# Performance work log

Measured on AMD Instinct MI355X. Metric: run time of the kernel, lower is better.

## Reference

```python
import jax, jax.numpy as jnp
import numpy as np
import math

H = 16        # num_heads
HD = 64       # head_dim


def get_slopes(n):
    def pow2(n):
        start = 2 ** (-2 ** (-(math.log2(n) - 3)))
        return [start * start ** i for i in range(n)]
    if math.log2(n).is_integer():
        return pow2(n)
    c = 2 ** math.floor(math.log2(n))
    return pow2(c) + get_slopes(2 * c)[0::2][: n - c]


def setup_inputs() -> dict:
    key = jax.random.key(0)
    ks = jax.random.split(key, 6)
    b, n, d = 2, 2048, 1024
    s = 1.0 / math.sqrt(d)
    return {
        "x": jax.random.normal(ks[0], (b, n, d), jnp.float32),
        "Wq": jax.random.normal(ks[1], (d, d), jnp.float32) * s,
        "Wk": jax.random.normal(ks[2], (d, d), jnp.float32) * s,
        "Wv": jax.random.normal(ks[3], (d, d), jnp.float32) * s,
        "Wo": jax.random.normal(ks[4], (d, d), jnp.float32) * s,
        "bo": jnp.zeros((d,), jnp.float32),
    }


def reference(x, Wq, Wk, Wv, Wo, bo):
    b, n, d = x.shape
    # project and split heads: [b, H, n, HD]
    def heads(w):
        return (x @ w).reshape(b, n, H, HD).transpose(0, 2, 1, 3)
    q, k, v = heads(Wq), heads(Wk), heads(Wv)

    scores = jnp.einsum("bhqd,bhkd->bhqk", q, k)  # [b,H,n,n]
    pos = jnp.arange(n)
    dist = jnp.abs(pos[None, :] - pos[:, None]).astype(scores.dtype)  # [n,n]
    slopes = jnp.asarray(get_slopes(H), dtype=scores.dtype)
    scores = scores - slopes[:, None, None] * dist  # alibi subtracted BEFORE scaling (as in source)
    causal = pos[None, :] > pos[:, None]            # upper triangle masked
    scores = jnp.where(causal, -jnp.inf, scores)
    attn = jax.nn.softmax(scores / math.sqrt(HD), axis=-1)
    ctx = jnp.einsum("bhqk,bhkd->bhqd", attn, v)
    ctx = ctx.transpose(0, 2, 1, 3).reshape(b, n, d)
    return ctx @ Wo + bo
```

## Files before the change

kernel.cpp:

```cpp
#include <hip/hip_runtime.h>
#include <hip/hip_bf16.h>
#include <stdint.h>

#define NH 16
#define HDIM 64
#define NB 2
#define NSEQ 2048
#define DM 1024
#define MROWS (NB * NSEQ)

typedef __attribute__((ext_vector_type(8))) short bf16x8;
typedef __attribute__((ext_vector_type(4))) float f32x4;

#define MFMA32(a, b, c) __builtin_amdgcn_mfma_f32_16x16x32_bf16(a, b, c, 0, 0, 0)

static __device__ __forceinline__ unsigned short f2bf(float f) {
    union { float f; unsigned u; } v;
    v.f = f;
    unsigned r = v.u + 0x7fffu + ((v.u >> 16) & 1u);
    return (unsigned short)(r >> 16);
}

static __device__ __forceinline__ unsigned pack2bf(float a, float b) {
#if __has_builtin(__builtin_amdgcn_cvt_pk_bf16_f32)
    typedef __attribute__((ext_vector_type(2))) __bf16 bf2_t;
    union { bf2_t v; unsigned u; } c;
    c.v = __builtin_amdgcn_cvt_pk_bf16_f32(a, b);
    return c.u;
#else
    return (unsigned)f2bf(a) | ((unsigned)f2bf(b) << 16);
#endif
}

static __device__ __forceinline__ float fexp2(float x) {
#if __has_builtin(__builtin_amdgcn_exp2f)
    return __builtin_amdgcn_exp2f(x);
#else
    return exp2f(x);
#endif
}

typedef __attribute__((address_space(1))) void* gas_ptr;
typedef __attribute__((address_space(3))) void* las_ptr;

static __device__ __forceinline__ void load16_lds(const void* g, void* l) {
    __builtin_amdgcn_global_load_lds((gas_ptr)(uintptr_t)g, (las_ptr)(uintptr_t)l,
                                     16, 0, 0);
}

__global__ __launch_bounds__(256) void convert_kernel(
    const float* __restrict__ x,
    const float* __restrict__ wq, const float* __restrict__ wk,
    const float* __restrict__ wv, const float* __restrict__ wo,
    unsigned short* __restrict__ xb,
    unsigned short* __restrict__ wqkvt,
    unsigned short* __restrict__ wot)
{
    __shared__ unsigned short Ts[64][66];
    int t = threadIdx.x;
    int bx = blockIdx.x;
    if (bx < 1024) {
        const float4* xs = (const float4*)x + (long)bx * 1024;
        unsigned short* xd = xb + (long)bx * 4096;
#pragma unroll
        for (int i = 0; i < 4; i++) {
            float4 v = xs[i * 256 + t];
            ushort4 o;
            o.x = f2bf(v.x); o.y = f2bf(v.y); o.z = f2bf(v.z); o.w = f2bf(v.w);
            *(ushort4*)(xd + (i * 256 + t) * 4) = o;
        }
        return;
    }
    int wi = bx - 1024;
    int wsel = wi >> 8;
    int tile = wi & 255;
    int k0 = (tile >> 4) * 64, c0 = (tile & 15) * 64;
    const float* w = (wsel == 0) ? wq : (wsel == 1) ? wk : (wsel == 2) ? wv : wo;
    int lr = t >> 6, lc = t & 63;
#pragma unroll
    for (int rr = 0; rr < 16; rr++) {
        int row = rr * 4 + lr;
        Ts[row][lc] = f2bf(w[(long)(k0 + row) * DM + c0 + lc]);
    }
    __syncthreads();
    unsigned short* dst = (wsel == 3) ? wot : (wqkvt + (long)wsel * DM * DM);
#pragma unroll
    for (int rr = 0; rr < 16; rr++) {
        int crow = rr * 4 + lr;
        dst[(long)(c0 + crow) * DM + k0 + lc] = Ts[lc][crow];
    }
}

template<int MR>
static __device__ __forceinline__ void gemm_core_db(
    const unsigned short* __restrict__ A,
    const unsigned short* __restrict__ Bt,
    int m0, int n0,
    unsigned short* __restrict__ As,
    unsigned short* __restrict__ Bs,
    f32x4 (&acc)[MR][4])
{
    constexpr int MT  = MR * 32;
    constexpr int ASZ = MT * 32;
    constexpr int BSZ = 128 * 32;
    constexpr int NA  = MT / 64;

    int t = threadIdx.x;
    int lane = t & 63;
    int wave = t >> 6;
    int l16 = lane & 15, quad = lane >> 4;
    int wm = wave >> 1, wn = wave & 1;

    const char* gA[NA];
#pragma unroll
    for (int i = 0; i < NA; i++) {
        int b = i * 256 + t;
        int row = b >> 2, g = (b & 3) ^ ((row >> 1) & 3);
        gA[i] = (const char*)(A + (long)(m0 + row) * DM) + g * 16;
    }
    const char* gB[2];
#pragma unroll
    for (int i = 0; i < 2; i++) {
        int b = i * 256 + t;
        int row = b >> 2, g = (b & 3) ^ ((row >> 1) & 3);
        gB[i] = (const char*)(Bt + (long)(n0 + row) * DM) + g * 16;
    }

    int sread = quad ^ ((l16 >> 1) & 3);
    int faOff = (wm * (MT / 2) + l16) * 32 + sread * 8;
    int fbOff = (wn * 64 + l16) * 32 + sread * 8;

#pragma unroll
    for (int i = 0; i < NA; i++)
        load16_lds(gA[i], (char*)As + i * 4096 + t * 16);
#pragma unroll
    for (int i = 0; i < 2; i++)
        load16_lds(gB[i], (char*)Bs + i * 4096 + t * 16);

    for (int kk = 0; kk < DM; kk += 32) {
        int cur = (kk >> 5) & 1;
        __syncthreads();
        if (kk + 32 < DM) {
            int nxt = cur ^ 1;
            char* abuf = (char*)(As + nxt * ASZ);
            char* bbuf = (char*)(Bs + nxt * BSZ);
#pragma unroll
            for (int i = 0; i < NA; i++)
                load16_lds(gA[i] + (kk + 32) * 2, abuf + i * 4096 + t * 16);
#pragma unroll
            for (int i = 0; i < 2; i++)
                load16_lds(gB[i] + (kk + 32) * 2, bbuf + i * 4096 + t * 16);
        }
        const unsigned short* fa = As + cur * ASZ + faOff;
        const unsigned short* fb = Bs + cur * BSZ + fbOff;
        bf16x8 af[MR], bf[4];
#pragma unroll
        for (int r = 0; r < MR; r++) af[r] = *(const bf16x8*)(fa + r * 16 * 32);
#pragma unroll
        for (int c = 0; c < 4; c++) bf[c] = *(const bf16x8*)(fb + c * 16 * 32);
#pragma unroll
        for (int r = 0; r < MR; r++)
#pragma unroll
            for (int c = 0; c < 4; c++)
                acc[r][c] = MFMA32(af[r], bf[c], acc[r][c]);
    }
}

__global__ __launch_bounds__(256, 3) void qkv_gemm_kernel(
    const unsigned short* __restrict__ A,
    const unsigned short* __restrict__ Bt,
    unsigned short* __restrict__ Qo, unsigned short* __restrict__ Ko,
    unsigned short* __restrict__ Vt)
{
    __shared__ unsigned short As[2][128 * 32];
    __shared__ unsigned short Bs[2][128 * 32];
    __shared__ unsigned short Tw[4][16][72];

    f32x4 acc[4][4] = {};
    int id = blockIdx.y * 24 + blockIdx.x;
    id = (id & 7) * 96 + (id >> 3);
    int m0 = (id / 24) * 128, n0 = (id % 24) * 128;
    gemm_core_db<4>(A, Bt, m0, n0, &As[0][0], &Bs[0][0], acc);

    int t = threadIdx.x, wave = t >> 6, lane = t & 63;
    int l16 = lane & 15, quad = lane >> 4;
    int wm = wave >> 1, wn = wave & 1;
    int rg0 = m0 + wm * 64;
    int cg0 = n0 + wn * 64;
    int z = cg0 >> 10;
    int b_ = rg0 >> 11;
    int nb0 = rg0 & (NSEQ - 1);
    int h = (cg0 & 1023) >> 6;
    long bh = (long)(b_ * NH + h);

    if (z < 2) {
        unsigned short* dst = (z == 0 ? Qo : Ko) + bh * NSEQ * HDIM;
#pragma unroll
        for (int r = 0; r < 4; r++)
#pragma unroll
            for (int reg = 0; reg < 4; reg++) {
                long rowb = (long)(nb0 + r * 16 + quad * 4 + reg) * HDIM;
#pragma unroll
                for (int c = 0; c < 4; c++)
                    dst[rowb + c * 16 + l16] = f2bf(acc[r][c][reg]);
            }
    } else {
        unsigned short* dst = Vt + bh * HDIM * NSEQ;
#pragma unroll
        for (int c = 0; c < 4; c++) {
#pragma unroll
            for (int r = 0; r < 4; r++) {
                ushort4 u;
                u.x = f2bf(acc[r][c][0]); u.y = f2bf(acc[r][c][1]);
                u.z = f2bf(acc[r][c][2]); u.w = f2bf(acc[r][c][3]);
                *(ushort4*)&Tw[wave][l16][r * 16 + quad * 4] = u;
            }
#pragma unroll
            for (int j = 0; j < 4; j++) {
                int lrow = j * 4 + quad;
                ushort4 u = *(const ushort4*)&Tw[wave][lrow][l16 * 4];
                *(ushort4*)(dst + (long)(c * 16 + lrow) * NSEQ + nb0 + l16 * 4) = u;
            }
        }
    }
}

static __device__ __forceinline__ void softmax_fixed(
    f32x4* s, bool mask, int qb, int kb, float sc2, float mrow,
    f32x4& l_vec, unsigned pbu[2][4], int l16, int quad)
{
    if (mask) {
        int fdm = qb + l16 - kb - quad * 4;
#pragma unroll
        for (int tt = 0; tt < 4; tt++)
#pragma unroll
            for (int r = 0; r < 4; r++)
                if (tt * 16 + r > fdm) s[tt][r] = -3e38f;
    }
#pragma unroll
    for (int tt = 0; tt < 4; tt++)
#pragma unroll
        for (int r = 0; r < 4; r++)
            s[tt][r] = fexp2(s[tt][r] * sc2 - mrow);
#pragma unroll
    for (int r = 0; r < 4; r++)
        l_vec[r] += (s[0][r] + s[1][r]) + (s[2][r] + s[3][r]);

#pragma unroll
    for (int p = 0; p < 2; p++) {
        pbu[p][0] = pack2bf(s[2 * p][0],     s[2 * p][1]);
        pbu[p][1] = pack2bf(s[2 * p][2],     s[2 * p][3]);
        pbu[p][2] = pack2bf(s[2 * p + 1][0], s[2 * p + 1][1]);
        pbu[p][3] = pack2bf(s[2 * p + 1][2], s[2 * p + 1][3]);
    }
}

__global__ __launch_bounds__(512, 4) void attn_kernel(
    const unsigned short* __restrict__ Q,
    const unsigned short* __restrict__ K,
    const unsigned short* __restrict__ Vt,
    unsigned short* __restrict__ ctx)
{
    __shared__ unsigned short KV[2][16384];

    int t = threadIdx.x, w = t >> 6, lane = t & 63;
    int l16 = lane & 15, quad = lane >> 4;
    int r7 = l16 & 7;
    int bh = blockIdx.x;
    int b_ = bh >> 4, h = bh & 15;
    int pr = blockIdx.y;
    int t1 = 31 - pr, t0 = pr;
    bool isT0 = (w >= 4);
    int myTile = isT0 ? t0 : t1;
    int qb = myTile * 64 + (w & 3) * 16;
    int qlast = qb + 15;
    int nch = (t1 + 2) >> 1;

    const unsigned short* Kg  = K  + (long)bh * NSEQ * HDIM;
    const unsigned short* Vtg = Vt + (long)bh * HDIM * NSEQ;

    const float log2e = 1.44269504f;
    float slope = exp2f(-0.5f * (float)(h + 1));
    float sc2 = 0.125f * log2e;
    float ss2 = slope * sc2;

    const unsigned short* qp = Q + ((long)bh * NSEQ + qb + l16) * HDIM + quad * 8;
    bf16x8 aq0 = *(const bf16x8*)qp;
    bf16x8 aq1 = *(const bf16x8*)(qp + 32);

    f32x4 ci4;
#pragma unroll
    for (int r = 0; r < 4; r++)
        ci4[r] = slope * (float)(quad * 4 + r);
    float s16 = slope * 16.0f;

    f32x4 lv = {};
    f32x4 o[4] = {};

    int row = t >> 3, sp = t & 7, sw = sp ^ (row & 7);
    const unsigned short* gk = Kg + row * HDIM + sw * 8;
    const unsigned short* gv = Vtg + (long)row * NSEQ + sw * 8;

    {
        unsigned short* buf = KV[0];
        load16_lds(gk,             buf + t * 8);
        load16_lds(gk + 64 * HDIM, buf + 4096 + t * 8);
        load16_lds(gv,             buf + 8192 + t * 8);
        load16_lds(gv + 64,        buf + 12288 + t * 8);
    }

    for (int c = 0; c < nch; c++) {
        __syncthreads();
        if (c + 1 < nch) {
            int kb2 = (c + 1) * 128;
            unsigned short* buf = KV[(c + 1) & 1];
            load16_lds(gk + (long)kb2 * HDIM,        buf + t * 8);
            load16_lds(gk + (long)(kb2 + 64) * HDIM, buf + 4096 + t * 8);
            load16_lds(gv + kb2,                     buf + 8192 + t * 8);
            load16_lds(gv + kb2 + 64,                buf + 12288 + t * 8);
        }

#pragma unroll
        for (int hh = 0; hh < 2; hh++) {
            int kb = c * 128 + hh * 64;
            if (kb > qlast) continue;

            const unsigned short* Ks = KV[c & 1] + hh * 4096;
            const unsigned short* Vs = KV[c & 1] + 8192 + hh * 4096;

            f32x4 s[4];
            __builtin_amdgcn_s_setprio(1);
#pragma unroll
            for (int tt = 0; tt < 4; tt++) {
                int rr = tt * 16 + l16;
                bf16x8 k0 = *(const bf16x8*)(Ks + (rr * 8 + (quad ^ r7)) * 8);
                bf16x8 k1 = *(const bf16x8*)(Ks + (rr * 8 + ((quad + 4) ^ r7)) * 8);
                f32x4 cz;
#pragma unroll
                for (int r = 0; r < 4; r++)
                    cz[r] = ci4[r] + (float)tt * s16;
                f32x4 z = MFMA32(k0, aq0, cz);
                s[tt] = MFMA32(k1, aq1, z);
            }
            __builtin_amdgcn_s_setprio(0);

            float mrow = ss2 * (float)(qb + l16 - kb);
            unsigned pb[2][4];
            softmax_fixed(s, kb + 63 > qb, qb, kb, sc2, mrow, lv, pb, l16, quad);

            int q2 = quad >> 1, q1b = (quad & 1) << 3;
            __builtin_amdgcn_s_setprio(1);
#pragma unroll
            for (int cb = 0; cb < 4; cb++) {
                int rd = cb * 16 + l16;
                const char* vrow = (const char*)(Vs + rd * 64);
                int x7 = rd & 7;
#pragma unroll
                for (int p = 0; p < 2; p++) {
                    union { bf16x8 v; uint2 u2[2]; } a;
                    int sb0 = 4 * p + q2;
                    int sb1 = 4 * p + 2 + q2;
                    a.u2[0] = *(const uint2*)(vrow + ((sb0 ^ x7) << 4) + q1b);
                    a.u2[1] = *(const uint2*)(vrow + ((sb1 ^ x7) << 4) + q1b);
                    union { unsigned u[4]; bf16x8 v; } bv;
#pragma unroll
                    for (int i = 0; i < 4; i++) bv.u[i] = pb[p][i];
                    o[cb] = MFMA32(a.v, bv.v, o[cb]);
                }
            }
            __builtin_amdgcn_s_setprio(0);
        }
    }

    {
        float lt = (lv[0] + lv[1]) + (lv[2] + lv[3]);
        lt += __shfl_xor(lt, 16);
        lt += __shfl_xor(lt, 32);
        float inv = 1.0f / lt;
        long base = (((long)b_ * NSEQ + (qb + l16)) * NH + h) * HDIM + quad * 4;
#pragma unroll
        for (int cb = 0; cb < 4; cb++) {
            uint2 u;
            u.x = pack2bf(o[cb][0] * inv, o[cb][1] * inv);
            u.y = pack2bf(o[cb][2] * inv, o[cb][3] * inv);
            *(uint2*)(ctx + base + cb * 16) = u;
        }
    }
}

__global__ __launch_bounds__(256, 4) void out_gemm_kernel(
    const unsigned short* __restrict__ A,
    const unsigned short* __restrict__ Bt,
    const float* __restrict__ bias,
    float* __restrict__ out)
{
    __shared__ unsigned short As[2][64 * 32];
    __shared__ unsigned short Bs[2][128 * 32];
    f32x4 acc[2][4] = {};
    int id = blockIdx.y * 8 + blockIdx.x;
    id = (id & 7) * 64 + (id >> 3);
    int m0 = (id >> 3) * 64, n0 = (id & 7) * 128;
    gemm_core_db<2>(A, Bt, m0, n0, &As[0][0], &Bs[0][0], acc);

    int t = threadIdx.x, wave = t >> 6, lane = t & 63;
    int l16 = lane & 15, quad = lane >> 4;
    int wm = wave >> 1, wn = wave & 1;
    int rg0 = m0 + wm * 32, cg0 = n0 + wn * 64;
#pragma unroll
    for (int c = 0; c < 4; c++) {
        float bc = bias[cg0 + c * 16 + l16];
#pragma unroll
        for (int r = 0; r < 2; r++)
#pragma unroll
            for (int reg = 0; reg < 4; reg++)
                out[(long)(rg0 + r * 16 + quad * 4 + reg) * DM + cg0 + c * 16 + l16] =
                    acc[r][c][reg] + bc;
    }
}

extern "C" void kernel_launch(void* const* d_in, const int* in_sizes, int n_in,
                              void* d_out, int out_size, void* d_ws, size_t ws_size,
                              hipStream_t stream)
{
    const float* x  = (const float*)d_in[0];
    const float* wq = (const float*)d_in[1];
    const float* wk = (const float*)d_in[2];
    const float* wv = (const float*)d_in[3];
    const float* wo = (const float*)d_in[4];
    const float* bo = (const float*)d_in[5];

    char* ws = (char*)d_ws;
    unsigned short* xb    = (unsigned short*)(ws);
    unsigned short* wqkvt = (unsigned short*)(ws + (8L  << 20));
    unsigned short* wot   = (unsigned short*)(ws + (14L << 20));
    unsigned short* Qb    = (unsigned short*)(ws + (16L << 20));
    unsigned short* Kb    = (unsigned short*)(ws + (24L << 20));
    unsigned short* Vt    = (unsigned short*)(ws + (32L << 20));
    unsigned short* ctx   = (unsigned short*)(ws + (40L << 20));
    float* out = (float*)d_out;

    convert_kernel<<<2048, 256, 0, stream>>>(x, wq, wk, wv, wo, xb, wqkvt, wot);

    qkv_gemm_kernel<<<dim3(3 * DM / 128, MROWS / 128), 256, 0, stream>>>(
        xb, wqkvt, Qb, Kb, Vt);

    attn_kernel<<<dim3(NB * NH, 16), 512, 0, stream>>>(Qb, Kb, Vt, ctx);

    out_gemm_kernel<<<dim3(DM / 128, MROWS / 64), 256, 0, stream>>>(
        ctx, wot, bo, out);
}
```

Measured before the change: 165.8 us.

## Read V directly from global memory with permuted Vt layout, drop LDS staging

The projection kernel now writes V-transpose with a permuted column order, so each lane's 16-byte global load lines up with the P fragment layout of the MFMA. The attention kernel stops staging V in shared memory, halving the LDS buffer, and instead loads V fragments straight from global/L2 with software prefetch of the next column block. This cuts LDS traffic and footprint, which may allow more occupancy, but it adds global-load latency and redundant reads of V across the waves of a block.

```diff
diff --git a/kernel.cpp b/kernel.cpp
--- a/kernel.cpp
+++ b/kernel.cpp
@@ -206,6 +206,7 @@
             }
     } else {
         unsigned short* dst = Vt + bh * HDIM * NSEQ;
+        int vslot = (l16 >> 3) * 8 + (l16 & 3) * 2 + ((l16 >> 2) & 1);
 #pragma unroll
         for (int c = 0; c < 4; c++) {
 #pragma unroll
@@ -219,7 +220,7 @@
             for (int j = 0; j < 4; j++) {
                 int lrow = j * 4 + quad;
                 ushort4 u = *(const ushort4*)&Tw[wave][lrow][l16 * 4];
-                *(ushort4*)(dst + (long)(c * 16 + lrow) * NSEQ + nb0 + l16 * 4) = u;
+                *(ushort4*)(dst + (long)(c * 16 + lrow) * NSEQ + nb0 + vslot * 4) = u;
             }
         }
     }
@@ -261,7 +262,7 @@
     const unsigned short* __restrict__ Vt,
     unsigned short* __restrict__ ctx)
 {
-    __shared__ unsigned short KV[2][16384];
+    __shared__ unsigned short KV[2][8192];
 
     int t = threadIdx.x, w = t >> 6, lane = t & 63;
     int l16 = lane & 15, quad = lane >> 4;
@@ -270,8 +271,7 @@
     int b_ = bh >> 4, h = bh & 15;
     int pr = blockIdx.y;
     int t1 = 31 - pr, t0 = pr;
-    bool isT0 = (w >= 4);
-    int myTile = isT0 ? t0 : t1;
+    int myTile = (w >= 4) ? t0 : t1;
     int qb = myTile * 64 + (w & 3) * 16;
     int qlast = qb + 15;
     int nch = (t1 + 2) >> 1;
@@ -299,14 +299,11 @@
 
     int row = t >> 3, sp = t & 7, sw = sp ^ (row & 7);
     const unsigned short* gk = Kg + row * HDIM + sw * 8;
-    const unsigned short* gv = Vtg + (long)row * NSEQ + sw * 8;
 
     {
         unsigned short* buf = KV[0];
         load16_lds(gk,             buf + t * 8);
         load16_lds(gk + 64 * HDIM, buf + 4096 + t * 8);
-        load16_lds(gv,             buf + 8192 + t * 8);
-        load16_lds(gv + 64,        buf + 12288 + t * 8);
     }
 
     for (int c = 0; c < nch; c++) {
@@ -316,17 +313,14 @@
             unsigned short* buf = KV[(c + 1) & 1];
             load16_lds(gk + (long)kb2 * HDIM,        buf + t * 8);
             load16_lds(gk + (long)(kb2 + 64) * HDIM, buf + 4096 + t * 8);
-            load16_lds(gv + kb2,                     buf + 8192 + t * 8);
-            load16_lds(gv + kb2 + 64,                buf + 12288 + t * 8);
-        }
-
-#pragma unroll
+        }
+
+#pragma unroll 2
         for (int hh = 0; hh < 2; hh++) {
             int kb = c * 128 + hh * 64;
             if (kb > qlast) continue;
 
             const unsigned short* Ks = KV[c & 1] + hh * 4096;
-            const unsigned short* Vs = KV[c & 1] + 8192 + hh * 4096;
 
             f32x4 s[4];
             __builtin_amdgcn_s_setprio(1);
@@ -348,25 +342,29 @@
             unsigned pb[2][4];
             softmax_fixed(s, kb + 63 > qb, qb, kb, sc2, mrow, lv, pb, l16, quad);
 
-            int q2 = quad >> 1, q1b = (quad & 1) << 3;
+            const unsigned short* vbase = Vtg + kb;
             __builtin_amdgcn_s_setprio(1);
+            bf16x8 av0, av1;
+            {
+                const unsigned short* vr = vbase + (long)l16 * NSEQ;
+                av0 = *(const bf16x8*)(vr + quad * 8);
+                av1 = *(const bf16x8*)(vr + 32 + quad * 8);
+            }
 #pragma unroll
             for (int cb = 0; cb < 4; cb++) {
-                int rd = cb * 16 + l16;
-                const char* vrow = (const char*)(Vs + rd * 64);
-                int x7 = rd & 7;
-#pragma unroll
-                for (int p = 0; p < 2; p++) {
-                    union { bf16x8 v; uint2 u2[2]; } a;
-                    int sb0 = 4 * p + q2;
-                    int sb1 = 4 * p + 2 + q2;
-                    a.u2[0] = *(const uint2*)(vrow + ((sb0 ^ x7) << 4) + q1b);
-                    a.u2[1] = *(const uint2*)(vrow + ((sb1 ^ x7) << 4) + q1b);
-                    union { unsigned u[4]; bf16x8 v; } bv;
-#pragma unroll
-                    for (int i = 0; i < 4; i++) bv.u[i] = pb[p][i];
-                    o[cb] = MFMA32(a.v, bv.v, o[cb]);
+                bf16x8 n0 = av0, n1 = av1;
+                if (cb < 3) {
+                    const unsigned short* vr =
+                        vbase + (long)((cb + 1) * 16 + l16) * NSEQ;
+                    n0 = *(const bf16x8*)(vr + quad * 8);
+                    n1 = *(const bf16x8*)(vr + 32 + quad * 8);
                 }
+                union { unsigned u[4]; bf16x8 v; } b0, b1;
+#pragma unroll
+                for (int i = 0; i < 4; i++) { b0.u[i] = pb[0][i]; b1.u[i] = pb[1][i]; }
+                o[cb] = MFMA32(av0, b0.v, o[cb]);
+                o[cb] = MFMA32(av1, b1.v, o[cb]);
+                av0 = n0; av1 = n1;
             }
             __builtin_amdgcn_s_setprio(0);
         }
```

New measurement: 203.2 us. +22.6%, slower.

## Give each attention wave 32 query rows with half the threads per block

Applied to the files above, without the earlier changes.

The attention block shrinks from 512 to 256 threads, and each wave now handles two 16-row query sub-tiles instead of one. Every K and V fragment read from shared memory therefore feeds twice as many MFMAs, which cuts LDS read traffic per unit of compute. Each thread issues twice as many async K/V global-to-LDS loads to fill the same tile. The cost is higher register pressure from the doubled accumulators and scores, fewer waves per block to hide latency, and launch bounds lowered to 2 blocks.

```diff
diff --git a/kernel.cpp b/kernel.cpp
--- a/kernel.cpp
+++ b/kernel.cpp
@@ -255,7 +255,7 @@
     }
 }
 
-__global__ __launch_bounds__(512, 4) void attn_kernel(
+__global__ __launch_bounds__(256, 2) void attn_kernel(
     const unsigned short* __restrict__ Q,
     const unsigned short* __restrict__ K,
     const unsigned short* __restrict__ Vt,
@@ -270,10 +270,9 @@
     int b_ = bh >> 4, h = bh & 15;
     int pr = blockIdx.y;
     int t1 = 31 - pr, t0 = pr;
-    bool isT0 = (w >= 4);
-    int myTile = isT0 ? t0 : t1;
-    int qb = myTile * 64 + (w & 3) * 16;
-    int qlast = qb + 15;
+    int myTile = (w >= 2) ? t0 : t1;
+    int qb = myTile * 64 + (w & 1) * 32;
+    int qlast = qb + 31;
     int nch = (t1 + 2) >> 1;
 
     const unsigned short* Kg  = K  + (long)bh * NSEQ * HDIM;
@@ -284,9 +283,14 @@
     float sc2 = 0.125f * log2e;
     float ss2 = slope * sc2;
 
-    const unsigned short* qp = Q + ((long)bh * NSEQ + qb + l16) * HDIM + quad * 8;
-    bf16x8 aq0 = *(const bf16x8*)qp;
-    bf16x8 aq1 = *(const bf16x8*)(qp + 32);
+    bf16x8 aq0[2], aq1[2];
+#pragma unroll
+    for (int j = 0; j < 2; j++) {
+        const unsigned short* qp =
+            Q + ((long)bh * NSEQ + qb + j * 16 + l16) * HDIM + quad * 8;
+        aq0[j] = *(const bf16x8*)qp;
+        aq1[j] = *(const bf16x8*)(qp + 32);
+    }
 
     f32x4 ci4;
 #pragma unroll
@@ -294,8 +298,8 @@
         ci4[r] = slope * (float)(quad * 4 + r);
     float s16 = slope * 16.0f;
 
-    f32x4 lv = {};
-    f32x4 o[4] = {};
+    f32x4 lv[2] = {};
+    f32x4 o[2][4] = {};
 
     int row = t >> 3, sp = t & 7, sw = sp ^ (row & 7);
     const unsigned short* gk = Kg + row * HDIM + sw * 8;
@@ -303,10 +307,14 @@
 
     {
         unsigned short* buf = KV[0];
-        load16_lds(gk,             buf + t * 8);
-        load16_lds(gk + 64 * HDIM, buf + 4096 + t * 8);
-        load16_lds(gv,             buf + 8192 + t * 8);
-        load16_lds(gv + 64,        buf + 12288 + t * 8);
+        load16_lds(gk,                  buf + t * 8);
+        load16_lds(gk + 32 * HDIM,      buf + 2048  + t * 8);
+        load16_lds(gk + 64 * HDIM,      buf + 4096  + t * 8);
+        load16_lds(gk + 96 * HDIM,      buf + 6144  + t * 8);
+        load16_lds(gv,                  buf + 8192  + t * 8);
+        load16_lds(gv + 32 * NSEQ,      buf + 10240 + t * 8);
+        load16_lds(gv + 64,             buf + 12288 + t * 8);
+        load16_lds(gv + 64 + 32 * NSEQ, buf + 14336 + t * 8);
     }
 
     for (int c = 0; c < nch; c++) {
@@ -314,10 +322,16 @@
         if (c + 1 < nch) {
             int kb2 = (c + 1) * 128;
             unsigned short* buf = KV[(c + 1) & 1];
-            load16_lds(gk + (long)kb2 * HDIM,        buf + t * 8);
-            load16_lds(gk + (long)(kb2 + 64) * HDIM, buf + 4096 + t * 8);
-            load16_lds(gv + kb2,                     buf + 8192 + t * 8);
-            load16_lds(gv + kb2 + 64,                buf + 12288 + t * 8);
+            const unsigned short* kp = gk + (long)kb2 * HDIM;
+            const unsigned short* vp = gv + kb2;
+            load16_lds(kp,                  buf + t * 8);
+            load16_lds(kp + 32 * HDIM,      buf + 2048  + t * 8);
+            load16_lds(kp + 64 * HDIM,      buf + 4096  + t * 8);
+            load16_lds(kp + 96 * HDIM,      buf + 6144  + t * 8);
+            load16_lds(vp,                  buf + 8192  + t * 8);
+            load16_lds(vp + 32 * NSEQ,      buf + 10240 + t * 8);
+            load16_lds(vp + 64,             buf + 12288 + t * 8);
+            load16_lds(vp + 64 + 32 * NSEQ, buf + 14336 + t * 8);
         }
 
 #pragma unroll
@@ -328,7 +342,7 @@
             const unsigned short* Ks = KV[c & 1] + hh * 4096;
             const unsigned short* Vs = KV[c & 1] + 8192 + hh * 4096;
 
-            f32x4 s[4];
+            f32x4 s[2][4];
             __builtin_amdgcn_s_setprio(1);
 #pragma unroll
             for (int tt = 0; tt < 4; tt++) {
@@ -339,14 +353,21 @@
 #pragma unroll
                 for (int r = 0; r < 4; r++)
                     cz[r] = ci4[r] + (float)tt * s16;
-                f32x4 z = MFMA32(k0, aq0, cz);
-                s[tt] = MFMA32(k1, aq1, z);
+                f32x4 z0 = MFMA32(k0, aq0[0], cz);
+                s[0][tt] = MFMA32(k1, aq1[0], z0);
+                f32x4 z1 = MFMA32(k0, aq0[1], cz);
+                s[1][tt] = MFMA32(k1, aq1[1], z1);
             }
             __builtin_amdgcn_s_setprio(0);
 
-            float mrow = ss2 * (float)(qb + l16 - kb);
-            unsigned pb[2][4];
-            softmax_fixed(s, kb + 63 > qb, qb, kb, sc2, mrow, lv, pb, l16, quad);
+            unsigned pb[2][2][4];
+#pragma unroll
+            for (int j = 0; j < 2; j++) {
+                int qbj = qb + j * 16;
+                float mrow = ss2 * (float)(qbj + l16 - kb);
+                softmax_fixed(s[j], kb + 63 > qbj, qbj, kb, sc2, mrow,
+                              lv[j], pb[j], l16, quad);
+            }
 
             int q2 = quad >> 1, q1b = (quad & 1) << 3;
             __builtin_amdgcn_s_setprio(1);
@@ -362,27 +383,33 @@
                     int sb1 = 4 * p + 2 + q2;
                     a.u2[0] = *(const uint2*)(vrow + ((sb0 ^ x7) << 4) + q1b);
                     a.u2[1] = *(const uint2*)(vrow + ((sb1 ^ x7) << 4) + q1b);
-                    union { unsigned u[4]; bf16x8 v; } bv;
-#pragma unroll
-                    for (int i = 0; i < 4; i++) bv.u[i] = pb[p][i];
-                    o[cb] = MFMA32(a.v, bv.v, o[cb]);
+                    union { unsigned u[4]; bf16x8 v; } bv0, bv1;
+#pragma unroll
+                    for (int i = 0; i < 4; i++) {
+                        bv0.u[i] = pb[0][p][i];
+                        bv1.u[i] = pb[1][p][i];
+                    }
+                    o[0][cb] = MFMA32(a.v, bv0.v, o[0][cb]);
+                    o[1][cb] = MFMA32(a.v, bv1.v, o[1][cb]);
                 }
             }
             __builtin_amdgcn_s_setprio(0);
         }
     }
 
-    {
-        float lt = (lv[0] + lv[1]) + (lv[2] + lv[3]);
+#pragma unroll
+    for (int j = 0; j < 2; j++) {
+        float lt = (lv[j][0] + lv[j][1]) + (lv[j][2] + lv[j][3]);
         lt += __shfl_xor(lt, 16);
         lt += __shfl_xor(lt, 32);
         float inv = 1.0f / lt;
-        long base = (((long)b_ * NSEQ + (qb + l16)) * NH + h) * HDIM + quad * 4;
+        long base = (((long)b_ * NSEQ + (qb + j * 16 + l16)) * NH + h) * HDIM
+                    + quad * 4;
 #pragma unroll
         for (int cb = 0; cb < 4; cb++) {
             uint2 u;
-            u.x = pack2bf(o[cb][0] * inv, o[cb][1] * inv);
-            u.y = pack2bf(o[cb][2] * inv, o[cb][3] * inv);
+            u.x = pack2bf(o[j][cb][0] * inv, o[j][cb][1] * inv);
+            u.y = pack2bf(o[j][cb][2] * inv, o[j][cb][3] * inv);
             *(uint2*)(ctx + base + cb * 16) = u;
         }
     }
@@ -444,7 +471,7 @@
     qkv_gemm_kernel<<<dim3(3 * DM / 128, MROWS / 128), 256, 0, stream>>>(
         xb, wqkvt, Qb, Kb, Vt);
 
-    attn_kernel<<<dim3(NB * NH, 16), 512, 0, stream>>>(Qb, Kb, Vt, ctx);
+    attn_kernel<<<dim3(NB * NH, 16), 256, 0, stream>>>(Qb, Kb, Vt, ctx);
 
     out_gemm_kernel<<<dim3(DM / 128, MROWS / 64), 256, 0, stream>>>(
         ctx, wot, bo, out);
```

Measured after the change: 175.4 us. +5.8%, slower.
